# Kernel optimization log

Hardware: AMD Instinct MI355X
Metric: run time of the kernel (lower is better)

## Reference

```python
import jax, jax.numpy as jnp
import numpy as np

M = 1024       # molecules
A = 24         # atoms per molecule
N = M * A      # total atoms
H = 128        # hidden_channels
F = 128        # num_filters
G = 50         # num_gaussians
T = 3          # num_interactions
CUTOFF = 10.0
LOG2 = float(np.log(2.0))


def setup_inputs() -> dict:
    key = jax.random.key(0)
    ks = jax.random.split(key, 20)
    z = jax.random.randint(ks[0], (N,), 1, 10)
    # each molecule's atoms in a 5A box -> max pair dist 8.66 < cutoff, all pairs connected
    pos = jax.random.uniform(ks[1], (N, 3), dtype=jnp.float32) * 5.0
    batch = jnp.repeat(jnp.arange(M), A)
    # dense intra-molecule radius graph (deterministic shape)
    i = np.arange(A)
    s, d = np.meshgrid(i, i, indexing='ij')
    m = s != d
    s, d = s[m], d[m]                      # [A*(A-1)]
    offs = (np.arange(M) * A)[:, None]
    edge_index = jnp.asarray(np.stack([(offs + s[None]).ravel(),
                                       (offs + d[None]).ravel()]).astype(np.int64))
    nrm = lambda k, shape: jax.random.normal(k, shape, dtype=jnp.float32) * 0.05
    params = dict(
        emb=nrm(ks[2], (100, H)),
        mlp_w1=nrm(ks[3], (T, G, F)), mlp_b1=jnp.zeros((T, F), jnp.float32),
        mlp_w2=nrm(ks[4], (T, F, F)), mlp_b2=jnp.zeros((T, F), jnp.float32),
        lin1_w=nrm(ks[5], (T, H, F)),
        lin2_w=nrm(ks[6], (T, F, H)), lin2_b=jnp.zeros((T, H), jnp.float32),
        lin_w=nrm(ks[7], (T, H, H)), lin_b=jnp.zeros((T, H), jnp.float32),
        out_w1=nrm(ks[8], (H, H // 2)), out_b1=jnp.zeros((H // 2,), jnp.float32),
        out_w2=nrm(ks[9], (H // 2, 1)), out_b2=jnp.zeros((1,), jnp.float32),
    )
    return dict(z=z, pos=pos, batch=batch, edge_index=edge_index, **params)


def _ssp(x):  # shifted softplus
    return jax.nn.softplus(x) - LOG2


def reference(z, pos, batch, edge_index, emb,
              mlp_w1, mlp_b1, mlp_w2, mlp_b2,
              lin1_w, lin2_w, lin2_b, lin_w, lin_b,
              out_w1, out_b1, out_w2, out_b2):
    src, dst = edge_index[0], edge_index[1]          # message j->i: gather src, scatter dst
    h = emb[z]                                       # [N,H]
    diff = pos[src] - pos[dst]                       # [E,3]
    ew = jnp.sqrt(jnp.sum(diff * diff, axis=-1))     # [E] edge distances
    # Gaussian smearing
    offset = jnp.linspace(0.0, CUTOFF, G, dtype=jnp.float32)
    coeff = -0.5 / (offset[1] - offset[0]) ** 2
    ea = jnp.exp(coeff * (ew[:, None] - offset) ** 2)   # [E,G]
    # cosine cutoff
    C = 0.5 * (jnp.cos(ew * (np.pi / CUTOFF)) + 1.0)    # [E]
    for t in range(T):
        W = _ssp(ea @ mlp_w1[t] + mlp_b1[t]) @ mlp_w2[t] + mlp_b2[t]  # [E,F]
        W = W * C[:, None]
        xf = h @ lin1_w[t]                            # [N,F]
        msg = xf[src] * W                             # [E,F]
        agg = jax.ops.segment_sum(msg, dst, num_segments=N)  # [N,F]
        v = _ssp(agg @ lin2_w[t] + lin2_b[t]) @ lin_w[t] + lin_b[t]  # [N,H]
        h = h + v                                     # residual
    h = _ssp(h @ out_w1 + out_b1)                     # [N,H/2]
    atom_e = h @ out_w2 + out_b2                      # [N,1]
    return jax.ops.segment_sum(atom_e, batch, num_segments=M)  # [M,1] readout='add'
```

## Files before the change

### kernel.cpp

```cpp
#include <hip/hip_runtime.h>
#include <math.h>

#define AT 24
#define ATP 32
#define HD 128
#define GD 50
#define NT 3
#define CUTOFF 10.0f
#define NK 1024

#define KP_W 136
#define XFP 132

#define SZ_BIG (128*KP_W)
#define WS_LIN1(t) ((t)*SZ_BIG)
#define WS_LIN2(t) ((3+(t))*SZ_BIG)
#define WS_LIN(t)  ((6+(t))*SZ_BIG)
#define WS_OW1     (9*SZ_BIG)
#define WS_TAB     (9*SZ_BIG + 64*KP_W)

typedef __attribute__((ext_vector_type(8))) short short8;
typedef __attribute__((ext_vector_type(4))) float f32x4;
typedef __attribute__((ext_vector_type(2))) float f32x2;

__device__ __forceinline__ unsigned short f2bf(float x) {
    unsigned int u = __float_as_uint(x);
    return (unsigned short)((u + 0x7fffu + ((u >> 16) & 1u)) >> 16);
}
__device__ __forceinline__ float sspf(float x) {
    return fmaxf(x, 0.0f) + __logf(1.0f + __expf(-fabsf(x))) - 0.69314718055994531f;
}

__device__ __forceinline__ void g2l_async(const void* g, void* l, int bytes, int tid) {
    int w = tid >> 6, lane = tid & 63;
    const char* gc = (const char*)g + lane * 16;
    char* lc = (char*)l + lane * 16;
    for (int ofs = w * 1024; ofs < bytes; ofs += 8192) {
        __builtin_amdgcn_global_load_lds(
            (const __attribute__((address_space(1))) unsigned int*)(gc + ofs),
            (__attribute__((address_space(3))) unsigned int*)(lc + ofs), 16, 0, 0);
    }
}

__device__ __forceinline__ f32x4 mfma16(short8 a, short8 b, f32x4 c) {
    return __builtin_amdgcn_mfma_f32_16x16x32_bf16(a, b, c, 0, 0, 0);
}

template<int NKT>
__device__ __forceinline__ void gemm2(const unsigned short* A, const unsigned short* B,
                                      int q, f32x4* acc)
{
#pragma unroll
    for (int kt = 0; kt < NKT; ++kt) {
        short8 a  = *(const short8*)(A + kt * 32 + q * 8);
        short8 b0 = *(const short8*)(B + kt * 32 + q * 8);
        short8 b1 = *(const short8*)(B + 64 * KP_W + kt * 32 + q * 8);
        acc[0] = mfma16(a, b0, acc[0]);
        acc[1] = mfma16(a, b1, acc[1]);
    }
}

__global__ void __launch_bounds__(256) prep(
    const float* __restrict__ lin1_w, const float* __restrict__ lin2_w,
    const float* __restrict__ lin_w,  const float* __restrict__ out_w1,
    const float* __restrict__ mlp_w1, const float* __restrict__ mlp_b1,
    const float* __restrict__ mlp_w2, const float* __restrict__ mlp_b2,
    unsigned short* __restrict__ ws)
{
    int b = blockIdx.x, tid = threadIdx.x;
    if (b < 40) {
        const float* src; unsigned short* dst; int N, n0, rows;
        if (b < 36) {
            int mat = b >> 2, slice = b & 3;
            int grp = mat / 3, t = mat - grp * 3;
            const float* bases[3] = {lin1_w, lin2_w, lin_w};
            src = bases[grp] + t * HD * HD;
            dst = ws + (grp * 3 + t) * SZ_BIG;
            N = 128; n0 = slice * 32; rows = 32;
        } else {
            src = out_w1; dst = ws + WS_OW1; N = 64; n0 = (b - 36) * 16; rows = 16;
        }
        int nn = tid & 31, kk = tid >> 5;
        if (nn < rows) {
            for (int k = kk; k < KP_W; k += 8) {
                float v = (k < HD) ? src[k * N + n0 + nn] : 0.f;
                dst[(n0 + nn) * KP_W + k] = f2bf(v);
            }
        }
        return;
    }
    __shared__ __align__(16) float w2s[HD * HD];
    __shared__ __align__(16) float ea[9][52];
    __shared__ float pacc[4][5][128];
    __shared__ __align__(16) unsigned short tabst[8 * 256];

    int b2 = b - 40;
    int t = b2 >> 7, k0 = (b2 & 127) << 3;

    {
        const char* gc = (const char*)(mlp_w2 + t * HD * HD) + tid * 16;
        char* lc = (char*)w2s + tid * 16;
#pragma unroll
        for (int ofs = 0; ofs < 65536; ofs += 4096)
            __builtin_amdgcn_global_load_lds(
                (const __attribute__((address_space(1))) unsigned int*)(gc + ofs),
                (__attribute__((address_space(3))) unsigned int*)(lc + ofs), 16, 0, 0);
    }

    const float h = CUTOFF / (NK - 1);
    const float STEP = CUTOFF / (GD - 1);
    const float COEFF = -0.5f / (STEP * STEP);
    for (int i = tid; i < 9 * GD; i += 256) {
        int rr = i / GD, g = i - rr * GD;
        int k = min(k0 + rr, NK - 1);
        float r = (float)k * h;
        float d = r - (float)g * STEP;
        ea[rr][g] = __expf(COEFF * d * d);
    }
    __syncthreads();

    int j = tid & 127, kh = tid >> 7;
    float pre[5];
    float bb1 = mlp_b1[t * HD + j];
#pragma unroll
    for (int rr = 0; rr < 5; ++rr) pre[rr] = bb1;
    const float* w1p = mlp_w1 + t * GD * HD + j;
    for (int g0 = 0; g0 < 48; g0 += 4) {
        f32x4 e[5];
#pragma unroll
        for (int rr = 0; rr < 5; ++rr) e[rr] = *(const f32x4*)&ea[kh * 4 + rr][g0];
        float wv[4];
#pragma unroll
        for (int gg = 0; gg < 4; ++gg) wv[gg] = w1p[(g0 + gg) * HD];
#pragma unroll
        for (int gg = 0; gg < 4; ++gg)
#pragma unroll
            for (int rr = 0; rr < 5; ++rr)
                pre[rr] = fmaf(e[rr][gg], wv[gg], pre[rr]);
    }
#pragma unroll
    for (int g = 48; g < GD; ++g) {
        float wv = w1p[g * HD];
#pragma unroll
        for (int rr = 0; rr < 5; ++rr)
            pre[rr] = fmaf(ea[kh * 4 + rr][g], wv, pre[rr]);
    }
#pragma unroll
    for (int rr = 0; rr < 5; ++rr) pre[rr] = sspf(pre[rr]);

    {
        int wv_ = tid >> 6, l = tid & 63;
        int ubase = (wv_ & 1) << 6;
        float a0[5], a1[5];
#pragma unroll
        for (int rr = 0; rr < 5; ++rr) { a0[rr] = 0.f; a1[rr] = 0.f; }
#pragma unroll 8
        for (int step = 0; step < 64; ++step) {
            int uu = ubase + step;
            float wa = w2s[uu * HD + l];
            float wb = w2s[uu * HD + l + 64];
#pragma unroll
            for (int rr = 0; rr < 5; ++rr) {
                float hv = __uint_as_float(
                    __builtin_amdgcn_readlane(__float_as_uint(pre[rr]), step));
                a0[rr] = fmaf(hv, wa, a0[rr]);
                a1[rr] = fmaf(hv, wb, a1[rr]);
            }
        }
#pragma unroll
        for (int rr = 0; rr < 5; ++rr) {
            pacc[wv_][rr][l] = a0[rr];
            pacc[wv_][rr][l + 64] = a1[rr];
        }
    }
    __syncthreads();
    float bb2 = mlp_b2[t * HD + j];
    float Tv[5];
#pragma unroll
    for (int rr = 0; rr < 5; ++rr) {
        float s = pacc[2 * kh][rr][j] + pacc[2 * kh + 1][rr][j] + bb2;
        int k = min(k0 + kh * 4 + rr, NK - 1);
        float r = (float)k * h;
        Tv[rr] = s * 0.5f * (__cosf(r * 0.31415926535897931f) + 1.0f);
    }
#pragma unroll
    for (int rr = 0; rr < 4; ++rr) {
        int kr = kh * 4 + rr;
        int ofs = kr * 256 + (j >> 1) * 4 + (j & 1);
        tabst[ofs]     = f2bf(Tv[rr]);
        tabst[ofs + 2] = f2bf(Tv[rr + 1] - Tv[rr]);
    }
    __syncthreads();
    unsigned short* tb = ws + WS_TAB + (size_t)t * NK * 256 + k0 * 256;
    *(short8*)(tb + tid * 8) = *(const short8*)(tabst + tid * 8);
}

extern "C" __global__ __launch_bounds__(512, 4)
void schnet_tab(const int* __restrict__ z, const float* __restrict__ pos,
                const float* __restrict__ emb,
                const float* __restrict__ lin2_b, const float* __restrict__ lin_b,
                const float* __restrict__ out_b1, const float* __restrict__ out_w2,
                const float* __restrict__ out_b2,
                const unsigned short* __restrict__ ws,
                float* __restrict__ out)
{
    __shared__ __align__(16) unsigned char uni_s[ATP * XFP * 4];
    __shared__ __align__(16) unsigned short hb_s[ATP * KP_W];
    __shared__ __align__(16) unsigned short aggb_s[ATP * KP_W];
    __shared__ __align__(16) unsigned short wbuf_s[SZ_BIG];
    __shared__ uint2 ef_s[AT * AT];
    __shared__ float pos_s[AT * 4];
    __shared__ float lb2_s[NT * HD], lb_s[NT * HD];
    __shared__ float ob1_s[64], ow2_s[64];
    __shared__ float red_s;
    float* xf_s = (float*)uni_s;
    unsigned short* tmp_s = (unsigned short*)uni_s;

    const int tid = threadIdx.x, m = blockIdx.x, base = m * AT;
    const int w = tid >> 6, lane = tid & 63, q = lane >> 4, lm = lane & 15;
    const int rn = w & 1, cn = w >> 1;

    g2l_async(ws + WS_LIN1(0), wbuf_s, SZ_BIG * 2, tid);

    if (tid < AT * 3) pos_s[(tid / 3) * 4 + tid % 3] = pos[base * 3 + tid];
    if (tid < NT * HD) { lb2_s[tid] = lin2_b[tid]; lb_s[tid] = lin_b[tid]; }
    else if (tid < NT * HD + 64) ob1_s[tid - NT * HD] = out_b1[tid - NT * HD];
    else if (tid < NT * HD + 128) ow2_s[tid - NT * HD - 64] = out_w2[tid - NT * HD - 64];
    if (tid == 0) red_s = 0.f;
    float hreg[2][4];
#pragma unroll
    for (int c = 0; c < 2; ++c)
#pragma unroll
        for (int i = 0; i < 4; ++i) {
            int row = rn * 16 + q * 4 + i, col = cn * 16 + c * 64 + lm;
            float v = (row < AT) ? emb[z[base + row] * HD + col] : 0.f;
            hreg[c][i] = v;
            hb_s[row * KP_W + col] = f2bf(v);
        }
    for (int i = tid; i < 8 * HD; i += 512)
        aggb_s[(24 + (i >> 7)) * KP_W + (i & 127)] = 0;
    __syncthreads();
    const float INVH = (float)(NK - 1) / CUTOFF;
    for (int i = tid; i < AT * AT; i += 512) {
        int a = i / AT, s = i - a * AT;
        unsigned off; float f;
        if (a == s) { off = 1023u << 9; f = 0.f; }
        else {
            float dx = pos_s[s * 4 + 0] - pos_s[a * 4 + 0];
            float dy = pos_s[s * 4 + 1] - pos_s[a * 4 + 1];
            float dz = pos_s[s * 4 + 2] - pos_s[a * 4 + 2];
            float u = sqrtf(dx * dx + dy * dy + dz * dz) * INVH;
            int idx = (int)u;
            f = u - (float)idx;
            off = (unsigned)idx << 9;
        }
        uint2 ef; ef.x = off; ef.y = __float_as_uint(f);
        ef_s[i] = ef;
    }

    for (int t = 0; t < NT; ++t) {
        __syncthreads();
        {
            f32x4 acc[2] = {};
            gemm2<4>(&hb_s[(rn * 16 + lm) * KP_W], &wbuf_s[(cn * 16 + lm) * KP_W], q, acc);
#pragma unroll
            for (int c = 0; c < 2; ++c) {
                int col = cn * 16 + c * 64 + lm;
#pragma unroll
                for (int i = 0; i < 4; ++i)
                    xf_s[(rn * 16 + q * 4 + i) * XFP + col] = acc[c][i];
            }
        }
        __syncthreads();
        g2l_async(ws + WS_LIN2(t), wbuf_s, SZ_BIG * 2, tid);
        {
            const char* tb = (const char*)(ws + WS_TAB) + (size_t)t * (NK * 512);
            const int vlo = lane * 8;
            f32x2 ag[3] = {{0.f, 0.f}, {0.f, 0.f}, {0.f, 0.f}};
#pragma unroll 1
            for (int s0 = 0; s0 < AT; s0 += 6) {
                uint2 pk[3][6]; float fb[3][6]; f32x2 xv[6];
#pragma unroll
                for (int ss = 0; ss < 6; ++ss) {
                    int s = s0 + ss;
                    xv[ss] = *(const f32x2*)&xf_s[s * XFP + lane * 2];
#pragma unroll
                    for (int r = 0; r < 3; ++r) {
                        int a = w + 8 * r;
                        uint2 ef = ef_s[a * AT + s];
                        fb[r][ss] = __uint_as_float(ef.y);
                        pk[r][ss] = *(const uint2*)(tb + (ef.x + vlo));
                    }
                }
#pragma unroll
                for (int ss = 0; ss < 6; ++ss) {
#pragma unroll
                    for (int r = 0; r < 3; ++r) {
                        uint2 p = pk[r][ss];
                        f32x2 t01, d01;
                        t01.x = __uint_as_float(p.x << 16);
                        t01.y = __uint_as_float(p.x & 0xFFFF0000u);
                        d01.x = __uint_as_float(p.y << 16);
                        d01.y = __uint_as_float(p.y & 0xFFFF0000u);
                        f32x2 w01 = t01 + fb[r][ss] * d01;
                        ag[r] += w01 * xv[ss];
                    }
                }
            }
#pragma unroll
            for (int r = 0; r < 3; ++r) {
                int a = w + 8 * r;
                unsigned pkk = ((unsigned)f2bf(ag[r].y) << 16) | (unsigned)f2bf(ag[r].x);
                *(unsigned*)&aggb_s[a * KP_W + lane * 2] = pkk;
            }
        }
        __syncthreads();
        short8 lf[2][4];
        {
            const unsigned short* lwp = ws + WS_LIN(t);
#pragma unroll
            for (int c = 0; c < 2; ++c)
#pragma unroll
                for (int kt = 0; kt < 4; ++kt)
                    lf[c][kt] = *(const short8*)(lwp + (cn * 16 + c * 64 + lm) * KP_W + kt * 32 + q * 8);
        }
        {
            f32x4 acc[2] = {};
            gemm2<4>(&aggb_s[(rn * 16 + lm) * KP_W], &wbuf_s[(cn * 16 + lm) * KP_W], q, acc);
#pragma unroll
            for (int c = 0; c < 2; ++c) {
                int col = cn * 16 + c * 64 + lm;
                float bb = lb2_s[t * HD + col];
#pragma unroll
                for (int i = 0; i < 4; ++i)
                    tmp_s[(rn * 16 + q * 4 + i) * KP_W + col] = f2bf(sspf(acc[c][i] + bb));
            }
        }
        __syncthreads();
        if (t < NT - 1) g2l_async(ws + WS_LIN1(t + 1), wbuf_s, SZ_BIG * 2, tid);
        else            g2l_async(ws + WS_OW1, wbuf_s, 64 * KP_W * 2, tid);
        {
            f32x4 acc[2] = {};
            const unsigned short* A = &tmp_s[(rn * 16 + lm) * KP_W];
#pragma unroll
            for (int kt = 0; kt < 4; ++kt) {
                short8 a = *(const short8*)(A + kt * 32 + q * 8);
                acc[0] = mfma16(a, lf[0][kt], acc[0]);
                acc[1] = mfma16(a, lf[1][kt], acc[1]);
            }
#pragma unroll
            for (int c = 0; c < 2; ++c) {
                int col = cn * 16 + c * 64 + lm;
                float bb = lb_s[t * HD + col];
#pragma unroll
                for (int i = 0; i < 4; ++i) {
                    int row = rn * 16 + q * 4 + i;
                    float nh = hreg[c][i] + acc[c][i] + bb;
                    hreg[c][i] = nh;
                    hb_s[row * KP_W + col] = f2bf(nh);
                }
            }
        }
    }

    __syncthreads();
    {
        int rt = w & 1, co = w >> 1;
        int j = co * 16 + lm;
        f32x4 acc = {};
        const unsigned short* A = &hb_s[(rt * 16 + lm) * KP_W];
        const unsigned short* B = &wbuf_s[j * KP_W];
#pragma unroll
        for (int kt = 0; kt < 4; ++kt)
            acc = mfma16(*(const short8*)(A + kt * 32 + q * 8),
                         *(const short8*)(B + kt * 32 + q * 8), acc);
        float sum = 0.f;
        float bb = ob1_s[j], wo = ow2_s[j];
#pragma unroll
        for (int i = 0; i < 4; ++i) {
            int row = rt * 16 + q * 4 + i;
            if (row < AT) sum += sspf(acc[i] + bb) * wo;
        }
        for (int off = 32; off > 0; off >>= 1) sum += __shfl_down(sum, off);
        if (lane == 0) atomicAdd(&red_s, sum);
    }
    __syncthreads();
    if (tid == 0) out[m] = red_s + (float)AT * out_b2[0];
}

extern "C" void kernel_launch(void* const* d_in, const int* in_sizes, int n_in,
                              void* d_out, int out_size, void* d_ws, size_t ws_size,
                              hipStream_t stream) {
    const int*   z    = (const int*)  d_in[0];
    const float* pos  = (const float*)d_in[1];
    const float* emb  = (const float*)d_in[4];
    const float* mw1  = (const float*)d_in[5];
    const float* mb1  = (const float*)d_in[6];
    const float* mw2  = (const float*)d_in[7];
    const float* mb2  = (const float*)d_in[8];
    const float* l1w  = (const float*)d_in[9];
    const float* l2w  = (const float*)d_in[10];
    const float* l2b  = (const float*)d_in[11];
    const float* lw   = (const float*)d_in[12];
    const float* lb   = (const float*)d_in[13];
    const float* ow1  = (const float*)d_in[14];
    const float* ob1  = (const float*)d_in[15];
    const float* ow2  = (const float*)d_in[16];
    const float* ob2  = (const float*)d_in[17];

    unsigned short* ws = (unsigned short*)d_ws;

    prep<<<dim3(424), dim3(256), 0, stream>>>(l1w, l2w, lw, ow1, mw1, mb1, mw2, mb2, ws);
    schnet_tab<<<dim3(1024), dim3(512), 0, stream>>>(
        z, pos, emb, l2b, lb, ob1, ow2, ob2, ws, (float*)d_out);
}
```

Baseline: 182.8 us.

## Software-pipeline filter table gathers and use bf16 dot2 for interpolation

Table entries are re-laid out so each 32-bit word holds a (value, delta) bf16 pair, and the fractional weight is packed as (1, f) in bf16. Interpolation then becomes a single fdot2 per channel. The table gathers are issued early in a three-buffer rotation, with the first batch overlapping the lin1 GEMM, to hide global load latency. Offsets are made wave-uniform through readfirstlane. The trade-offs are higher register pressure from 36 live uint2 values per thread and a fractional weight rounded to bf16, which lowers interpolation precision.

```diff
diff --git a/kernel.cpp b/kernel.cpp
--- a/kernel.cpp
+++ b/kernel.cpp
@@ -30,6 +30,21 @@
 __device__ __forceinline__ float sspf(float x) {
     return fmaxf(x, 0.0f) + __logf(1.0f + __expf(-fabsf(x))) - 0.69314718055994531f;
 }
+
+#if __has_builtin(__builtin_amdgcn_fdot2_f32_bf16)
+typedef __attribute__((ext_vector_type(2))) __bf16 bfv2;
+__device__ __forceinline__ float dot2bf(unsigned td, unsigned fp) {
+    return __builtin_amdgcn_fdot2_f32_bf16(
+        __builtin_bit_cast(bfv2, td), __builtin_bit_cast(bfv2, fp), 0.0f, false);
+}
+#else
+__device__ __forceinline__ float dot2bf(unsigned td, unsigned fp) {
+    float t = __uint_as_float(td << 16);
+    float d = __uint_as_float(td & 0xFFFF0000u);
+    float f = __uint_as_float(fp & 0xFFFF0000u);
+    return fmaf(f, d, t);
+}
+#endif
 
 __device__ __forceinline__ void g2l_async(const void* g, void* l, int bytes, int tid) {
     int w = tid >> 6, lane = tid & 63;
@@ -186,14 +201,35 @@
 #pragma unroll
     for (int rr = 0; rr < 4; ++rr) {
         int kr = kh * 4 + rr;
-        int ofs = kr * 256 + (j >> 1) * 4 + (j & 1);
+        int ofs = kr * 256 + (j >> 1) * 4 + (j & 1) * 2;
         tabst[ofs]     = f2bf(Tv[rr]);
-        tabst[ofs + 2] = f2bf(Tv[rr + 1] - Tv[rr]);
+        tabst[ofs + 1] = f2bf(Tv[rr + 1] - Tv[rr]);
     }
     __syncthreads();
     unsigned short* tb = ws + WS_TAB + (size_t)t * NK * 256 + k0 * 256;
     *(short8*)(tb + tid * 8) = *(const short8*)(tabst + tid * 8);
 }
+
+#define ELOAD(P, s0) \
+    { _Pragma("unroll") \
+      for (int ss = 0; ss < 4; ++ss) { \
+        _Pragma("unroll") \
+        for (int r = 0; r < 3; ++r) { \
+            int off = __builtin_amdgcn_readfirstlane((int)eoff_s[(w + 8*r)*AT + (s0)+ss]); \
+            P[ss*3+r] = *(const uint2*)(tbase + off + vlo); \
+        } } }
+
+#define ECOMP(P, s0) \
+    { _Pragma("unroll") \
+      for (int ss = 0; ss < 4; ++ss) { \
+        f32x2 xv = *(const f32x2*)&xf_s[((s0)+ss)*XFP + lane*2]; \
+        _Pragma("unroll") \
+        for (int r = 0; r < 3; ++r) { \
+            unsigned fp = efpk_s[(w + 8*r)*AT + (s0)+ss]; \
+            uint2 p = P[ss*3+r]; \
+            ag[r].x = fmaf(dot2bf(p.x, fp), xv.x, ag[r].x); \
+            ag[r].y = fmaf(dot2bf(p.y, fp), xv.y, ag[r].y); \
+        } } }
 
 extern "C" __global__ __launch_bounds__(512, 4)
 void schnet_tab(const int* __restrict__ z, const float* __restrict__ pos,
@@ -208,7 +244,8 @@
     __shared__ __align__(16) unsigned short hb_s[ATP * KP_W];
     __shared__ __align__(16) unsigned short aggb_s[ATP * KP_W];
     __shared__ __align__(16) unsigned short wbuf_s[SZ_BIG];
-    __shared__ uint2 ef_s[AT * AT];
+    __shared__ unsigned eoff_s[AT * AT];
+    __shared__ unsigned efpk_s[AT * AT];
     __shared__ float pos_s[AT * 4];
     __shared__ float lb2_s[NT * HD], lb_s[NT * HD];
     __shared__ float ob1_s[64], ow2_s[64];
@@ -254,12 +291,17 @@
             f = u - (float)idx;
             off = (unsigned)idx << 9;
         }
-        uint2 ef; ef.x = off; ef.y = __float_as_uint(f);
-        ef_s[i] = ef;
+        eoff_s[i] = off;
+        efpk_s[i] = 0x3F80u | ((unsigned)f2bf(f) << 16);
     }
 
     for (int t = 0; t < NT; ++t) {
         __syncthreads();
+        const char* tbase = (const char*)(ws + WS_TAB) + (size_t)t * (NK * 512);
+        const int vlo = lane * 8;
+        uint2 pA[12], pB[12], pC[12];
+        f32x2 ag[3] = {{0.f, 0.f}, {0.f, 0.f}, {0.f, 0.f}};
+        ELOAD(pA, 0);
         {
             f32x4 acc[2] = {};
             gemm2<4>(&hb_s[(rn * 16 + lm) * KP_W], &wbuf_s[(cn * 16 + lm) * KP_W], q, acc);
@@ -272,47 +314,20 @@
             }
         }
         __syncthreads();
+        ELOAD(pB, 4);
+        ELOAD(pC, 8);
         g2l_async(ws + WS_LIN2(t), wbuf_s, SZ_BIG * 2, tid);
-        {
-            const char* tb = (const char*)(ws + WS_TAB) + (size_t)t * (NK * 512);
-            const int vlo = lane * 8;
-            f32x2 ag[3] = {{0.f, 0.f}, {0.f, 0.f}, {0.f, 0.f}};
-#pragma unroll 1
-            for (int s0 = 0; s0 < AT; s0 += 6) {
-                uint2 pk[3][6]; float fb[3][6]; f32x2 xv[6];
-#pragma unroll
-                for (int ss = 0; ss < 6; ++ss) {
-                    int s = s0 + ss;
-                    xv[ss] = *(const f32x2*)&xf_s[s * XFP + lane * 2];
-#pragma unroll
-                    for (int r = 0; r < 3; ++r) {
-                        int a = w + 8 * r;
-                        uint2 ef = ef_s[a * AT + s];
-                        fb[r][ss] = __uint_as_float(ef.y);
-                        pk[r][ss] = *(const uint2*)(tb + (ef.x + vlo));
-                    }
-                }
-#pragma unroll
-                for (int ss = 0; ss < 6; ++ss) {
-#pragma unroll
-                    for (int r = 0; r < 3; ++r) {
-                        uint2 p = pk[r][ss];
-                        f32x2 t01, d01;
-                        t01.x = __uint_as_float(p.x << 16);
-                        t01.y = __uint_as_float(p.x & 0xFFFF0000u);
-                        d01.x = __uint_as_float(p.y << 16);
-                        d01.y = __uint_as_float(p.y & 0xFFFF0000u);
-                        f32x2 w01 = t01 + fb[r][ss] * d01;
-                        ag[r] += w01 * xv[ss];
-                    }
-                }
-            }
-#pragma unroll
-            for (int r = 0; r < 3; ++r) {
-                int a = w + 8 * r;
-                unsigned pkk = ((unsigned)f2bf(ag[r].y) << 16) | (unsigned)f2bf(ag[r].x);
-                *(unsigned*)&aggb_s[a * KP_W + lane * 2] = pkk;
-            }
+        ECOMP(pA, 0);   ELOAD(pA, 12);
+        ECOMP(pB, 4);   ELOAD(pB, 16);
+        ECOMP(pC, 8);   ELOAD(pC, 20);
+        ECOMP(pA, 12);
+        ECOMP(pB, 16);
+        ECOMP(pC, 20);
+#pragma unroll
+        for (int r = 0; r < 3; ++r) {
+            int a = w + 8 * r;
+            unsigned pkk = ((unsigned)f2bf(ag[r].y) << 16) | (unsigned)f2bf(ag[r].x);
+            *(unsigned*)&aggb_s[a * KP_W + lane * 2] = pkk;
         }
         __syncthreads();
         short8 lf[2][4];
```

New measurement: 202.9 us. 1.11x slower.

## Drop LDS weight staging, load weights directly to registers, use bf16 dot2 interpolation

Applied to the files above, without the earlier changes.

Removes the 34KB LDS weight buffer and the async global-to-LDS weight copies, so every GEMM now loads its B fragments straight from global/L2 into registers. The bias arrays are read from global memory instead of being staged in LDS. The smaller LDS footprint, together with launch bounds raised to 8 blocks per CU, is meant to allow more resident blocks per CU. The edge table is interleaved as (value, delta) pairs and the interpolation becomes one bf16 fdot2 per channel, with the per-edge offset and fraction made wave-uniform via readfirstlane. The trade-off is more global/L2 traffic per block, tighter register limits from the higher occupancy target, and a bf16-rounded fraction.

```diff
diff --git a/kernel.cpp b/kernel.cpp
--- a/kernel.cpp
+++ b/kernel.cpp
@@ -31,33 +31,32 @@
     return fmaxf(x, 0.0f) + __logf(1.0f + __expf(-fabsf(x))) - 0.69314718055994531f;
 }
 
-__device__ __forceinline__ void g2l_async(const void* g, void* l, int bytes, int tid) {
-    int w = tid >> 6, lane = tid & 63;
-    const char* gc = (const char*)g + lane * 16;
-    char* lc = (char*)l + lane * 16;
-    for (int ofs = w * 1024; ofs < bytes; ofs += 8192) {
-        __builtin_amdgcn_global_load_lds(
-            (const __attribute__((address_space(1))) unsigned int*)(gc + ofs),
-            (__attribute__((address_space(3))) unsigned int*)(lc + ofs), 16, 0, 0);
-    }
-}
+#if __has_builtin(__builtin_amdgcn_fdot2_f32_bf16)
+typedef __attribute__((ext_vector_type(2))) __bf16 bfv2;
+__device__ __forceinline__ float dot2bf(unsigned td, unsigned fp) {
+    return __builtin_amdgcn_fdot2_f32_bf16(
+        __builtin_bit_cast(bfv2, td), __builtin_bit_cast(bfv2, fp), 0.0f, false);
+}
+#else
+__device__ __forceinline__ float dot2bf(unsigned td, unsigned fp) {
+    float t = __uint_as_float(td << 16);
+    float d = __uint_as_float(td & 0xFFFF0000u);
+    float f = __uint_as_float(fp & 0xFFFF0000u);
+    return fmaf(f, d, t);
+}
+#endif
 
 __device__ __forceinline__ f32x4 mfma16(short8 a, short8 b, f32x4 c) {
     return __builtin_amdgcn_mfma_f32_16x16x32_bf16(a, b, c, 0, 0, 0);
 }
 
-template<int NKT>
-__device__ __forceinline__ void gemm2(const unsigned short* A, const unsigned short* B,
-                                      int q, f32x4* acc)
-{
-#pragma unroll
-    for (int kt = 0; kt < NKT; ++kt) {
-        short8 a  = *(const short8*)(A + kt * 32 + q * 8);
-        short8 b0 = *(const short8*)(B + kt * 32 + q * 8);
-        short8 b1 = *(const short8*)(B + 64 * KP_W + kt * 32 + q * 8);
-        acc[0] = mfma16(a, b0, acc[0]);
-        acc[1] = mfma16(a, b1, acc[1]);
-    }
+__device__ __forceinline__ void loadB(const unsigned short* __restrict__ Bp,
+                                      int cn, int lm, int q, short8 (&bf)[2][4]) {
+#pragma unroll
+    for (int c = 0; c < 2; ++c)
+#pragma unroll
+        for (int kt = 0; kt < 4; ++kt)
+            bf[c][kt] = *(const short8*)(Bp + (cn * 16 + c * 64 + lm) * KP_W + kt * 32 + q * 8);
 }
 
 __global__ void __launch_bounds__(256) prep(
@@ -186,16 +185,16 @@
 #pragma unroll
     for (int rr = 0; rr < 4; ++rr) {
         int kr = kh * 4 + rr;
-        int ofs = kr * 256 + (j >> 1) * 4 + (j & 1);
+        int ofs = kr * 256 + (j >> 1) * 4 + (j & 1) * 2;
         tabst[ofs]     = f2bf(Tv[rr]);
-        tabst[ofs + 2] = f2bf(Tv[rr + 1] - Tv[rr]);
+        tabst[ofs + 1] = f2bf(Tv[rr + 1] - Tv[rr]);
     }
     __syncthreads();
     unsigned short* tb = ws + WS_TAB + (size_t)t * NK * 256 + k0 * 256;
     *(short8*)(tb + tid * 8) = *(const short8*)(tabst + tid * 8);
 }
 
-extern "C" __global__ __launch_bounds__(512, 4)
+extern "C" __global__ __launch_bounds__(512, 8)
 void schnet_tab(const int* __restrict__ z, const float* __restrict__ pos,
                 const float* __restrict__ emb,
                 const float* __restrict__ lin2_b, const float* __restrict__ lin_b,
@@ -207,11 +206,9 @@
     __shared__ __align__(16) unsigned char uni_s[ATP * XFP * 4];
     __shared__ __align__(16) unsigned short hb_s[ATP * KP_W];
     __shared__ __align__(16) unsigned short aggb_s[ATP * KP_W];
-    __shared__ __align__(16) unsigned short wbuf_s[SZ_BIG];
-    __shared__ uint2 ef_s[AT * AT];
+    __shared__ unsigned eoff_s[AT * AT];
+    __shared__ unsigned efpk_s[AT * AT];
     __shared__ float pos_s[AT * 4];
-    __shared__ float lb2_s[NT * HD], lb_s[NT * HD];
-    __shared__ float ob1_s[64], ow2_s[64];
     __shared__ float red_s;
     float* xf_s = (float*)uni_s;
     unsigned short* tmp_s = (unsigned short*)uni_s;
@@ -220,12 +217,7 @@
     const int w = tid >> 6, lane = tid & 63, q = lane >> 4, lm = lane & 15;
     const int rn = w & 1, cn = w >> 1;
 
-    g2l_async(ws + WS_LIN1(0), wbuf_s, SZ_BIG * 2, tid);
-
     if (tid < AT * 3) pos_s[(tid / 3) * 4 + tid % 3] = pos[base * 3 + tid];
-    if (tid < NT * HD) { lb2_s[tid] = lin2_b[tid]; lb_s[tid] = lin_b[tid]; }
-    else if (tid < NT * HD + 64) ob1_s[tid - NT * HD] = out_b1[tid - NT * HD];
-    else if (tid < NT * HD + 128) ow2_s[tid - NT * HD - 64] = out_w2[tid - NT * HD - 64];
     if (tid == 0) red_s = 0.f;
     float hreg[2][4];
 #pragma unroll
@@ -254,15 +246,23 @@
             f = u - (float)idx;
             off = (unsigned)idx << 9;
         }
-        uint2 ef; ef.x = off; ef.y = __float_as_uint(f);
-        ef_s[i] = ef;
+        eoff_s[i] = off;
+        efpk_s[i] = 0x3F80u | ((unsigned)f2bf(f) << 16);
     }
 
     for (int t = 0; t < NT; ++t) {
         __syncthreads();
         {
+            short8 bf[2][4];
+            loadB(ws + WS_LIN1(t), cn, lm, q, bf);
             f32x4 acc[2] = {};
-            gemm2<4>(&hb_s[(rn * 16 + lm) * KP_W], &wbuf_s[(cn * 16 + lm) * KP_W], q, acc);
+            const unsigned short* A = &hb_s[(rn * 16 + lm) * KP_W];
+#pragma unroll
+            for (int kt = 0; kt < 4; ++kt) {
+                short8 a = *(const short8*)(A + kt * 32 + q * 8);
+                acc[0] = mfma16(a, bf[0][kt], acc[0]);
+                acc[1] = mfma16(a, bf[1][kt], acc[1]);
+            }
 #pragma unroll
             for (int c = 0; c < 2; ++c) {
                 int col = cn * 16 + c * 64 + lm;
@@ -272,14 +272,13 @@
             }
         }
         __syncthreads();
-        g2l_async(ws + WS_LIN2(t), wbuf_s, SZ_BIG * 2, tid);
         {
-            const char* tb = (const char*)(ws + WS_TAB) + (size_t)t * (NK * 512);
+            const char* tbase = (const char*)(ws + WS_TAB) + (size_t)t * (NK * 512);
             const int vlo = lane * 8;
             f32x2 ag[3] = {{0.f, 0.f}, {0.f, 0.f}, {0.f, 0.f}};
 #pragma unroll 1
             for (int s0 = 0; s0 < AT; s0 += 6) {
-                uint2 pk[3][6]; float fb[3][6]; f32x2 xv[6];
+                uint2 pk[3][6]; unsigned fp[3][6]; f32x2 xv[6];
 #pragma unroll
                 for (int ss = 0; ss < 6; ++ss) {
                     int s = s0 + ss;
@@ -287,9 +286,9 @@
 #pragma unroll
                     for (int r = 0; r < 3; ++r) {
                         int a = w + 8 * r;
-                        uint2 ef = ef_s[a * AT + s];
-                        fb[r][ss] = __uint_as_float(ef.y);
-                        pk[r][ss] = *(const uint2*)(tb + (ef.x + vlo));
+                        int off = __builtin_amdgcn_readfirstlane((int)eoff_s[a * AT + s]);
+                        fp[r][ss] = __builtin_amdgcn_readfirstlane(efpk_s[a * AT + s]);
+                        pk[r][ss] = *(const uint2*)(tbase + off + vlo);
                     }
                 }
 #pragma unroll
@@ -297,13 +296,8 @@
 #pragma unroll
                     for (int r = 0; r < 3; ++r) {
                         uint2 p = pk[r][ss];
-                        f32x2 t01, d01;
-                        t01.x = __uint_as_float(p.x << 16);
-                        t01.y = __uint_as_float(p.x & 0xFFFF0000u);
-                        d01.x = __uint_as_float(p.y << 16);
-                        d01.y = __uint_as_float(p.y & 0xFFFF0000u);
-                        f32x2 w01 = t01 + fb[r][ss] * d01;
-                        ag[r] += w01 * xv[ss];
+                        ag[r].x = fmaf(dot2bf(p.x, fp[r][ss]), xv[ss].x, ag[r].x);
+                        ag[r].y = fmaf(dot2bf(p.y, fp[r][ss]), xv[ss].y, ag[r].y);
                     }
                 }
             }
@@ -316,29 +310,28 @@
         }
         __syncthreads();
         short8 lf[2][4];
+        loadB(ws + WS_LIN(t), cn, lm, q, lf);
         {
-            const unsigned short* lwp = ws + WS_LIN(t);
-#pragma unroll
-            for (int c = 0; c < 2; ++c)
-#pragma unroll
-                for (int kt = 0; kt < 4; ++kt)
-                    lf[c][kt] = *(const short8*)(lwp + (cn * 16 + c * 64 + lm) * KP_W + kt * 32 + q * 8);
-        }
-        {
+            short8 bf[2][4];
+            loadB(ws + WS_LIN2(t), cn, lm, q, bf);
             f32x4 acc[2] = {};
-            gemm2<4>(&aggb_s[(rn * 16 + lm) * KP_W], &wbuf_s[(cn * 16 + lm) * KP_W], q, acc);
+            const unsigned short* A = &aggb_s[(rn * 16 + lm) * KP_W];
+#pragma unroll
+            for (int kt = 0; kt < 4; ++kt) {
+                short8 a = *(const short8*)(A + kt * 32 + q * 8);
+                acc[0] = mfma16(a, bf[0][kt], acc[0]);
+                acc[1] = mfma16(a, bf[1][kt], acc[1]);
+            }
 #pragma unroll
             for (int c = 0; c < 2; ++c) {
                 int col = cn * 16 + c * 64 + lm;
-                float bb = lb2_s[t * HD + col];
+                float bb = lin2_b[t * HD + col];
 #pragma unroll
                 for (int i = 0; i < 4; ++i)
                     tmp_s[(rn * 16 + q * 4 + i) * KP_W + col] = f2bf(sspf(acc[c][i] + bb));
             }
         }
         __syncthreads();
-        if (t < NT - 1) g2l_async(ws + WS_LIN1(t + 1), wbuf_s, SZ_BIG * 2, tid);
-        else            g2l_async(ws + WS_OW1, wbuf_s, 64 * KP_W * 2, tid);
         {
             f32x4 acc[2] = {};
             const unsigned short* A = &tmp_s[(rn * 16 + lm) * KP_W];
@@ -351,7 +344,7 @@
 #pragma unroll
             for (int c = 0; c < 2; ++c) {
                 int col = cn * 16 + c * 64 + lm;
-                float bb = lb_s[t * HD + col];
+                float bb = lin_b[t * HD + col];
 #pragma unroll
                 for (int i = 0; i < 4; ++i) {
                     int row = rn * 16 + q * 4 + i;
@@ -367,15 +360,18 @@
     {
         int rt = w & 1, co = w >> 1;
         int j = co * 16 + lm;
+        short8 bh[4];
+        const unsigned short* Bp = ws + WS_OW1 + j * KP_W;
+#pragma unroll
+        for (int kt = 0; kt < 4; ++kt)
+            bh[kt] = *(const short8*)(Bp + kt * 32 + q * 8);
         f32x4 acc = {};
         const unsigned short* A = &hb_s[(rt * 16 + lm) * KP_W];
-        const unsigned short* B = &wbuf_s[j * KP_W];
 #pragma unroll
         for (int kt = 0; kt < 4; ++kt)
-            acc = mfma16(*(const short8*)(A + kt * 32 + q * 8),
-                         *(const short8*)(B + kt * 32 + q * 8), acc);
+            acc = mfma16(*(const short8*)(A + kt * 32 + q * 8), bh[kt], acc);
         float sum = 0.f;
-        float bb = ob1_s[j], wo = ow2_s[j];
+        float bb = out_b1[j], wo = out_w2[j];
 #pragma unroll
         for (int i = 0; i < 4; ++i) {
             int row = rt * 16 + q * 4 + i;
```

Result: slower. 259.4 us (+41.9%).
